# Optimization experiments

Hardware: AMD Instinct MI355X
Metric: run time of the kernel (lower is better)

## Reference

```python
import jax, jax.numpy as jnp
import numpy as np

B = 131072
D = 256
N_SC = 16
SC_CAP = 2
MAX_USERS = 8
POW_DIM = 10


def setup_inputs() -> dict:
    key = jax.random.key(0)
    k0, k1, k2, k3 = jax.random.split(key, 4)
    x = jax.random.normal(k0, (B, D), dtype=jnp.float32)
    available_actions = jax.random.randint(k1, (B, 2 * MAX_USERS), 0, 2).astype(jnp.int32)
    # per-head Categorical weights: Linear(D, action_dim), small init (gain=0.01 orthogonal-ish)
    W_sc = jax.random.normal(k2, (MAX_USERS, D, N_SC), dtype=jnp.float32) * 0.01
    b_sc = jnp.zeros((MAX_USERS, N_SC), dtype=jnp.float32)
    W_pow = jax.random.normal(k3, (MAX_USERS, D, POW_DIM), dtype=jnp.float32) * 0.01
    b_pow = jnp.zeros((MAX_USERS, POW_DIM), dtype=jnp.float32)
    return {"x": x, "available_actions": available_actions,
            "W_sc": W_sc, "b_sc": b_sc, "W_pow": W_pow, "b_pow": b_pow}


def reference(x, available_actions, W_sc, b_sc, W_pow, b_pow):
    # NOMA branch of MultiDiscreteACTLayer.forward (deterministic=False).
    Bn = x.shape[0]
    key = jax.random.key(42)
    sc_keys = jax.random.split(key, MAX_USERS)
    pow_key = jax.random.fold_in(key, 999)

    NEG = jnp.float32(-1e10)

    def sc_step(sc_stat, inp):
        W, b, avail, k = inp  # W:[D,N_SC], b:[N_SC], avail:[Bn] float, k: key
        logits = x @ W + b                       # [Bn, N_SC]
        mask = sc_stat < SC_CAP                  # subchannel still has capacity
        logits = jnp.where(mask, logits, NEG)
        action = jax.random.categorical(k, logits)        # [Bn] int
        logp = jnp.take_along_axis(jax.nn.log_softmax(logits, -1),
                                   action[:, None], axis=-1)[:, 0]
        # availability masking: unavailable -> action=-1, logp=0
        action = jnp.where(avail > 0, action, -1)
        logp = logp * avail
        # scatter: sc_stat[b, action] += 1 where action != -1
        upd = jnp.where((action >= 0)[:, None],
                        jax.nn.one_hot(jnp.maximum(action, 0), N_SC, dtype=sc_stat.dtype),
                        jnp.zeros((), sc_stat.dtype))
        return sc_stat + upd, (action, logp)

    sc_stat0 = jnp.zeros((Bn, N_SC), dtype=x.dtype)
    avail_f = available_actions.astype(x.dtype)
    avail_sc = avail_f[:, :MAX_USERS].T          # [MAX_USERS, Bn]
    _, (sc_actions, sc_logps) = jax.lax.scan(
        sc_step, sc_stat0, (W_sc, b_sc, avail_sc, sc_keys))

    # power heads: no mask, no loop-carried state -> fully batched
    pow_logits = jnp.einsum('bd,hdk->bhk', x, W_pow) + b_pow   # [Bn, H, POW_DIM]
    pow_actions = jax.random.categorical(pow_key, pow_logits)  # [Bn, H]
    pow_logps = jnp.take_along_axis(jax.nn.log_softmax(pow_logits, -1),
                                    pow_actions[..., None], axis=-1)[..., 0]
    avail_pow = avail_f[:, MAX_USERS:]
    pow_actions = jnp.where(avail_pow > 0, pow_actions, -1)
    pow_logps = pow_logps * avail_pow

    actions = jnp.concatenate([sc_actions.T, pow_actions], axis=-1)          # [Bn, 16]
    action_log_probs = jnp.concatenate([sc_logps.T, pow_logps], axis=-1)
    action_log_probs = jnp.sum(action_log_probs, axis=-1, keepdims=True)     # [Bn, 1]
    return actions, action_log_probs, available_actions
```

## Files before the change

kernel.cpp:

```cpp
#include <hip/hip_runtime.h>


#define B_TOTAL 131072
#define NCOL    208
#define ROWS    32
#define TINYF   1.17549435e-38f

#define WPLANE  53248
#define XB_L    8448
#define XB_P    264

typedef float f32x4 __attribute__((ext_vector_type(4)));
typedef short short8 __attribute__((ext_vector_type(8)));

#define MFMA_BF16(A,B,C) __builtin_amdgcn_mfma_f32_16x16x32_bf16((A),(B),(C),0,0,0)

#define ROR16(v, n) __uint_as_float((unsigned)__builtin_amdgcn_update_dpp(     \
    (int)__float_as_uint(v), (int)__float_as_uint(v), 0x120 | (n), 0xF, 0xF, false))

__device__ __forceinline__ float redmax16(float v) {
  v = fmaxf(v, ROR16(v, 8));
  v = fmaxf(v, ROR16(v, 4));
  v = fmaxf(v, ROR16(v, 2));
  v = fmaxf(v, ROR16(v, 1));
  return v;
}
__device__ __forceinline__ float redsum16(float v) {
  v += ROR16(v, 8);
  v += ROR16(v, 4);
  v += ROR16(v, 2);
  v += ROR16(v, 1);
  return v;
}

struct TF2 { unsigned a, b; };

__host__ __device__ constexpr unsigned rotl_(unsigned x, int r) {
  return (x << r) | (x >> (32 - r));
}

__host__ __device__ constexpr TF2 tf2(unsigned k0, unsigned k1, unsigned x0, unsigned x1) {
  unsigned ks0 = k0, ks1 = k1, ks2 = k0 ^ k1 ^ 0x1BD11BDAu;
  x0 += ks0; x1 += ks1;
  x0 += x1; x1 = rotl_(x1, 13); x1 ^= x0;
  x0 += x1; x1 = rotl_(x1, 15); x1 ^= x0;
  x0 += x1; x1 = rotl_(x1, 26); x1 ^= x0;
  x0 += x1; x1 = rotl_(x1,  6); x1 ^= x0;
  x0 += ks1; x1 += ks2 + 1u;
  x0 += x1; x1 = rotl_(x1, 17); x1 ^= x0;
  x0 += x1; x1 = rotl_(x1, 29); x1 ^= x0;
  x0 += x1; x1 = rotl_(x1, 16); x1 ^= x0;
  x0 += x1; x1 = rotl_(x1, 24); x1 ^= x0;
  x0 += ks2; x1 += ks0 + 2u;
  x0 += x1; x1 = rotl_(x1, 13); x1 ^= x0;
  x0 += x1; x1 = rotl_(x1, 15); x1 ^= x0;
  x0 += x1; x1 = rotl_(x1, 26); x1 ^= x0;
  x0 += x1; x1 = rotl_(x1,  6); x1 ^= x0;
  x0 += ks0; x1 += ks1 + 3u;
  x0 += x1; x1 = rotl_(x1, 17); x1 ^= x0;
  x0 += x1; x1 = rotl_(x1, 29); x1 ^= x0;
  x0 += x1; x1 = rotl_(x1, 16); x1 ^= x0;
  x0 += x1; x1 = rotl_(x1, 24); x1 ^= x0;
  x0 += ks1; x1 += ks2 + 4u;
  x0 += x1; x1 = rotl_(x1, 13); x1 ^= x0;
  x0 += x1; x1 = rotl_(x1, 15); x1 ^= x0;
  x0 += x1; x1 = rotl_(x1, 26); x1 ^= x0;
  x0 += x1; x1 = rotl_(x1,  6); x1 ^= x0;
  x0 += ks2; x1 += ks0 + 5u;
  return TF2{x0, x1};
}

__host__ __device__ constexpr unsigned key_a(unsigned d) { return tf2(0u, 42u, 0u, d).a; }
__host__ __device__ constexpr unsigned key_b(unsigned d) { return tf2(0u, 42u, 0u, d).b; }

constexpr unsigned SK0c[8] = {
  key_a(0), key_a(1), key_a(2), key_a(3), key_a(4), key_a(5), key_a(6), key_a(7)
};
constexpr unsigned SK1c[8] = {
  key_b(0), key_b(1), key_b(2), key_b(3), key_b(4), key_b(5), key_b(6), key_b(7)
};
constexpr unsigned PK0 = key_a(999);
constexpr unsigned PK1 = key_b(999);

__device__ __forceinline__ double dlog(double xd) {
  long long b = __double_as_longlong(xd);
  int e = (int)(b >> 52) - 1023;
  double m = __longlong_as_double((b & 0x000FFFFFFFFFFFFFLL) | 0x3FF0000000000000LL);
  if (m > 1.4142135623730951) { m *= 0.5; e += 1; }
  double mp1 = m + 1.0;
  double r = (double)__builtin_amdgcn_rcpf((float)mp1);
  r = fma(fma(-mp1, r, 1.0), r, r);
  double z  = (m - 1.0) * r;
  double z2 = z * z;
  double p = fma(z2, fma(z2, fma(z2, fma(z2, fma(z2,
              1.0/13.0, 1.0/11.0), 1.0/9.0), 1.0/7.0), 1.0/5.0), 1.0/3.0);
  double lm = fma(2.0 * z, z2 * p, 2.0 * z);
  return fma((double)e, 0.6931471805599453, lm);
}

__device__ __forceinline__ float gumbelf(unsigned bits) {
  float u = __uint_as_float((bits >> 9) | 0x3f800000u) - 1.0f;
  u = u + TINYF;
  u = fmaxf(TINYF, u);
  double nl = -dlog((double)u);
  return -(float)dlog(nl);
}

__global__ void repack_kernel(const float* __restrict__ Wsc, const float* __restrict__ bsc,
                              const float* __restrict__ Wpow, const float* __restrict__ bpow,
                              short* __restrict__ Wb, float* __restrict__ bp) {
  int t = blockIdx.x * 256 + threadIdx.x;
  if (t < 53248) {
    int j    = t & 7;
    int lane = (t >> 3) & 63;
    int c    = (t >> 9) & 7;
    int T    = t >> 12;
    int k    = c * 32 + (lane >> 4) * 8 + j;
    int col  = T * 16 + (lane & 15);
    int u = col / 26, n = col % 26;
    float w = (n < 16) ? Wsc[(u * 256 + k) * 16 + n]
                       : Wpow[(u * 256 + k) * 10 + (n - 16)];
    unsigned b0 = __float_as_uint(w) & 0xFFFF0000u;
    float f1 = w - __uint_as_float(b0);
    unsigned b1 = __float_as_uint(f1) & 0xFFFF0000u;
    float f2 = f1 - __uint_as_float(b1);
    unsigned b2 = __float_as_uint(f2) & 0xFFFF0000u;
    int idx = (T * 8 + c) * 512 + lane * 8 + j;
    Wb[idx]              = (short)(b0 >> 16);
    Wb[WPLANE + idx]     = (short)(b1 >> 16);
    Wb[2 * WPLANE + idx] = (short)(b2 >> 16);
  } else {
    int cc = t - 53248;
    float v = 0.f;
    if (cc < NCOL) {
      int u = cc / 26, n = cc % 26;
      v = (n < 16) ? bsc[u * 16 + n] : bpow[u * 10 + (n - 16)];
    }
    bp[cc] = v;
  }
}

#define PROD8(X0, X1, X2, W0, W1, W2, AM, AS) do {                      \
    AM = MFMA_BF16(X0, W0, AM);                                         \
    AS = MFMA_BF16(X1, W0, AS);                                         \
    AS = MFMA_BF16(X0, W1, AS);                                         \
    AS = MFMA_BF16(X1, W1, AS);                                         \
    AS = MFMA_BF16(X2, W0, AS);                                         \
    AS = MFMA_BF16(X0, W2, AS);                                         \
    AS = MFMA_BF16(X2, W1, AS);                                         \
    AS = MFMA_BF16(X1, W2, AS);                                         \
  } while (0)

__global__ __launch_bounds__(512, 4) void act_kernel(
    const float* __restrict__ x, const int* __restrict__ avail,
    const short* __restrict__ Wb, const float* __restrict__ bp,
    float* __restrict__ out) {
  __shared__ __align__(16) union SMem {
    short xb[3][ROWS][XB_P];
    float gpow[ROWS][80];
  } sm;
  __shared__ float lg[ROWS][NCOL];

  const int t = threadIdx.x;
  const int b0 = blockIdx.x * ROWS;

#pragma unroll
  for (int i = 0; i < 4; ++i) {
    int flat = t + 512 * i;
    int r  = flat >> 6;
    int kq = flat & 63;
    float4 v = ((const float4*)(x + (size_t)(b0 + r) * 256))[kq];
    unsigned L0[4], L1[4], L2[4];
#pragma unroll
    for (int e = 0; e < 4; ++e) {
      float f = (&v.x)[e];
      unsigned h0 = __float_as_uint(f) & 0xFFFF0000u;
      float f1 = f - __uint_as_float(h0);
      unsigned h1 = __float_as_uint(f1) & 0xFFFF0000u;
      float f2 = f1 - __uint_as_float(h1);
      unsigned h2 = __float_as_uint(f2) & 0xFFFF0000u;
      L0[e] = h0; L1[e] = h1; L2[e] = h2;
    }
    int ks = 4 * kq;
    *(uint2*)&sm.xb[0][r][ks] =
        make_uint2((L0[0] >> 16) | (L0[1] & 0xFFFF0000u),
                   (L0[2] >> 16) | (L0[3] & 0xFFFF0000u));
    *(uint2*)&sm.xb[1][r][ks] =
        make_uint2((L1[0] >> 16) | (L1[1] & 0xFFFF0000u),
                   (L1[2] >> 16) | (L1[3] & 0xFFFF0000u));
    *(uint2*)&sm.xb[2][r][ks] =
        make_uint2((L2[0] >> 16) | (L2[1] & 0xFFFF0000u),
                   (L2[2] >> 16) | (L2[3] & 0xFFFF0000u));
  }
  __syncthreads();

  {
    const int lane64 = t & 63;
    const int wv  = t >> 6;
    const int q   = lane64 >> 4;
    const int r16 = lane64 & 15;
    const int tA  = (wv + (blockIdx.x & 7)) & 7;
    const bool heavy = tA < 5;
    const int tB  = 8 + tA;

    const f32x4 fz = {0.f, 0.f, 0.f, 0.f};
    f32x4 mA0 = fz, sA0 = fz, mA1 = fz, sA1 = fz;
    f32x4 mB0 = fz, sB0 = fz, mB1 = fz, sB1 = fz;

    const short* xr0 = &sm.xb[0][r16][0];
    const short* xr1 = &sm.xb[0][16 + r16][0];
    const int wlane = lane64 * 8;

#pragma unroll 1
    for (int c = 0; c < 8; ++c) {
      const int xo = c * 32 + q * 8;
      short8 a0 = *(const short8*)(xr0 + xo);
      short8 a1 = *(const short8*)(xr0 + XB_L + xo);
      short8 a2 = *(const short8*)(xr0 + 2 * XB_L + xo);
      short8 c0_ = *(const short8*)(xr1 + xo);
      short8 c1_ = *(const short8*)(xr1 + XB_L + xo);
      short8 c2_ = *(const short8*)(xr1 + 2 * XB_L + xo);
      {
        const int wi = (tA * 8 + c) * 512 + wlane;
        short8 w0 = *(const short8*)(Wb + wi);
        short8 w1 = *(const short8*)(Wb + WPLANE + wi);
        short8 w2 = *(const short8*)(Wb + 2 * WPLANE + wi);
        PROD8(a0,  a1,  a2,  w0, w1, w2, mA0, sA0);
        PROD8(c0_, c1_, c2_, w0, w1, w2, mA1, sA1);
      }
      if (heavy) {
        const int wi = (tB * 8 + c) * 512 + wlane;
        short8 w0 = *(const short8*)(Wb + wi);
        short8 w1 = *(const short8*)(Wb + WPLANE + wi);
        short8 w2 = *(const short8*)(Wb + 2 * WPLANE + wi);
        PROD8(a0,  a1,  a2,  w0, w1, w2, mB0, sB0);
        PROD8(c0_, c1_, c2_, w0, w1, w2, mB1, sB1);
      }
    }

    {
      short8 pa = {0, 0, 0, 0, 0, 0, 0, 0};
      short8 pb = {0, 0, 0, 0, 0, 0, 0, 0};
      if (q == 0) {
        pa[0] = (short)(__float_as_uint((float)r16) >> 16);
        pb[0] = (short)0x3F80;
      }
      f32x4 pr = MFMA_BF16(pa, pb, fz);
      f32x4 pc = MFMA_BF16(pb, pa, fz);
#pragma unroll
      for (int r = 0; r < 4; ++r) {
        int i  = ((int)(pr[r] + 0.5f)) & 15;
        int jo = ((int)(pc[r] + 0.5f)) & 15;
        int cA = tA * 16 + jo;
        lg[i][cA]      = mA0[r] + (sA0[r] + bp[cA]);
        lg[16 + i][cA] = mA1[r] + (sA1[r] + bp[cA]);
        if (heavy) {
          int cB = tB * 16 + jo;
          lg[i][cB]      = mB0[r] + (sB0[r] + bp[cB]);
          lg[16 + i][cB] = mB1[r] + (sB1[r] + bp[cB]);
        }
      }
    }
  }

  float gsc[8];
  {
    const int prow = t >> 4;
    const int pn   = t & 15;
    const unsigned cnt = (unsigned)((b0 + prow) * 16 + pn);
#pragma unroll
    for (int u = 0; u < 8; ++u) {
      TF2 r = tf2(SK0c[u], SK1c[u], 0u, cnt);
      gsc[u] = gumbelf(r.a ^ r.b);
    }
  }
  __syncthreads();

#pragma unroll
  for (int i = 0; i < 5; ++i) {
    int flat = t + 512 * i;
    int prw  = (flat * 13108) >> 20;
    int q80  = flat - prw * 80;
    unsigned cnt = (unsigned)((b0 + prw) * 80 + q80);
    TF2 r = tf2(PK0, PK1, 0u, cnt);
    sm.gpow[prw][q80] = gumbelf(r.a ^ r.b);
  }
  __syncthreads();

  const int row  = t >> 4;
  const int lane = t & 15;
  const int g16  = (t & 63) >> 4;
  const int shamt = g16 * 16;
  const int gb   = b0 + row;
  const int av = avail[gb * 16 + lane];
  const unsigned avm = (unsigned)((__ballot(av > 0) >> shamt) & 0xFFFFull);
  int stat = 0;
  float lpsum = 0.0f;
  float my_act = 0.0f;

#pragma unroll
  for (int u = 0; u < 8; ++u) {
    float logit = lg[row][u * 26 + lane];
    float ml = (stat < 2) ? logit : -1e10f;
    float y  = ml + gsc[u];
    float vmax = redmax16(y);
    unsigned long long bal = __ballot(y == vmax);
    int idx = __builtin_ctz((unsigned)((bal >> shamt) & 0xFFFFull));
    float s = redsum16(__expf(ml));
    float mlidx = redmax16((lane == idx) ? ml : -3.0e38f);
    float lp = mlidx - __logf(s);
    int au = (int)((avm >> u) & 1u);
    if (au) {
      lpsum += lp;
      if (lane == idx) stat += 1;
    }
    if (lane == u) my_act = au ? (float)idx : -1.0f;
  }

#pragma unroll
  for (int h = 0; h < 8; ++h) {
    bool on = lane < 10;
    float logit = on ? lg[row][h * 26 + 16 + lane] : -3.0e38f;
    float y     = on ? (logit + sm.gpow[row][h * 10 + lane]) : -3.0e38f;
    float vmax = redmax16(y);
    unsigned long long bal = __ballot(y == vmax);
    int idx = __builtin_ctz((unsigned)((bal >> shamt) & 0xFFFFull));
    float s = redsum16(on ? __expf(logit) : 0.0f);
    float mlidx = redmax16((lane == idx) ? logit : -3.0e38f);
    float lp = mlidx - __logf(s);
    int ah = (int)((avm >> (8 + h)) & 1u);
    if (ah) lpsum += lp;
    if (lane == 8 + h) my_act = ah ? (float)idx : -1.0f;
  }

  out[(size_t)gb * 16 + lane] = my_act;
  if (lane == 0) out[(size_t)B_TOTAL * 16 + gb] = lpsum;
  out[(size_t)B_TOTAL * 17 + (size_t)gb * 16 + lane] = (float)av;
}

extern "C" void kernel_launch(void* const* d_in, const int* in_sizes, int n_in,
                              void* d_out, int out_size, void* d_ws, size_t ws_size,
                              hipStream_t stream) {
  const float* x    = (const float*)d_in[0];
  const int*   av   = (const int*)  d_in[1];
  const float* Wsc  = (const float*)d_in[2];
  const float* bsc  = (const float*)d_in[3];
  const float* Wpow = (const float*)d_in[4];
  const float* bpow = (const float*)d_in[5];
  float* outp = (float*)d_out;

  float* bp = (float*)d_ws;
  short* Wb = (short*)((char*)d_ws + 1024);

  repack_kernel<<<209, 256, 0, stream>>>(Wsc, bsc, Wpow, bpow, Wb, bp);
  act_kernel<<<B_TOTAL / ROWS, 512, 0, stream>>>(x, av, Wb, bp, outp);
}
```

Measured before the change: 375.9 us.

## Alias transposed logits buffer into x staging LDS and raise occupancy target

Moves the logits scratch into the same shared-memory union as the bf16 x split buffers, stored transposed so each thread writes its four MFMA accumulator rows as one float4. This removes the separate logits allocation, so more blocks can share a CU's LDS, and launch bounds are raised from 4 to 6 blocks per CU. An extra barrier is added before overwriting the x buffers, and the subchannel Gumbel noise generation is moved after the logit stores. The higher occupancy target constrains registers and may cause spills, and the transposed reads may hit bank conflicts.

```diff
diff --git a/kernel.cpp b/kernel.cpp
--- a/kernel.cpp
+++ b/kernel.cpp
@@ -9,6 +9,7 @@
 #define WPLANE  53248
 #define XB_L    8448
 #define XB_P    264
+#define LGP     36
 
 typedef float f32x4 __attribute__((ext_vector_type(4)));
 typedef short short8 __attribute__((ext_vector_type(8)));
@@ -151,15 +152,17 @@
     AS = MFMA_BF16(X1, W2, AS);                                         \
   } while (0)
 
-__global__ __launch_bounds__(512, 4) void act_kernel(
+__global__ __launch_bounds__(512, 6) void act_kernel(
     const float* __restrict__ x, const int* __restrict__ avail,
     const short* __restrict__ Wb, const float* __restrict__ bp,
     float* __restrict__ out) {
   __shared__ __align__(16) union SMem {
     short xb[3][ROWS][XB_P];
-    float gpow[ROWS][80];
+    struct {
+      float gpow[ROWS][80];
+      float lgT[NCOL][LGP];
+    } c;
   } sm;
-  __shared__ float lg[ROWS][NCOL];
 
   const int t = threadIdx.x;
   const int b0 = blockIdx.x * ROWS;
@@ -194,16 +197,18 @@
   }
   __syncthreads();
 
+  const int lane64 = t & 63;
+  const int wv  = t >> 6;
+  const int q   = lane64 >> 4;
+  const int r16 = lane64 & 15;
+  const int tA  = (wv + (blockIdx.x & 7)) & 7;
+  const bool heavy = tA < 5;
+  const int tB  = 8 + tA;
+
+  const f32x4 fz = {0.f, 0.f, 0.f, 0.f};
+  f32x4 dA0, dA1, dB0, dB1;
+  int i0, jo;
   {
-    const int lane64 = t & 63;
-    const int wv  = t >> 6;
-    const int q   = lane64 >> 4;
-    const int r16 = lane64 & 15;
-    const int tA  = (wv + (blockIdx.x & 7)) & 7;
-    const bool heavy = tA < 5;
-    const int tB  = 8 + tA;
-
-    const f32x4 fz = {0.f, 0.f, 0.f, 0.f};
     f32x4 mA0 = fz, sA0 = fz, mA1 = fz, sA1 = fz;
     f32x4 mB0 = fz, sB0 = fz, mB1 = fz, sB1 = fz;
 
@@ -238,43 +243,39 @@
       }
     }
 
-    {
-      short8 pa = {0, 0, 0, 0, 0, 0, 0, 0};
-      short8 pb = {0, 0, 0, 0, 0, 0, 0, 0};
-      if (q == 0) {
-        pa[0] = (short)(__float_as_uint((float)r16) >> 16);
-        pb[0] = (short)0x3F80;
-      }
-      f32x4 pr = MFMA_BF16(pa, pb, fz);
-      f32x4 pc = MFMA_BF16(pb, pa, fz);
-#pragma unroll
-      for (int r = 0; r < 4; ++r) {
-        int i  = ((int)(pr[r] + 0.5f)) & 15;
-        int jo = ((int)(pc[r] + 0.5f)) & 15;
-        int cA = tA * 16 + jo;
-        lg[i][cA]      = mA0[r] + (sA0[r] + bp[cA]);
-        lg[16 + i][cA] = mA1[r] + (sA1[r] + bp[cA]);
-        if (heavy) {
-          int cB = tB * 16 + jo;
-          lg[i][cB]      = mB0[r] + (sB0[r] + bp[cB]);
-          lg[16 + i][cB] = mB1[r] + (sB1[r] + bp[cB]);
-        }
-      }
-    }
-  }
-
-  float gsc[8];
+    short8 pa = {0, 0, 0, 0, 0, 0, 0, 0};
+    short8 pb = {0, 0, 0, 0, 0, 0, 0, 0};
+    if (q == 0) {
+      pa[0] = (short)(__float_as_uint((float)r16) >> 16);
+      pb[0] = (short)0x3F80;
+    }
+    f32x4 pr = MFMA_BF16(pa, pb, fz);
+    f32x4 pc = MFMA_BF16(pb, pa, fz);
+    i0 = ((int)(pr[0] + 0.5f)) & 15;
+    jo = ((int)(pc[0] + 0.5f)) & 15;
+
+    dA0 = mA0 + sA0; dA1 = mA1 + sA1;
+    dB0 = mB0 + sB0; dB1 = mB1 + sB1;
+  }
+  __syncthreads();
+
   {
-    const int prow = t >> 4;
-    const int pn   = t & 15;
-    const unsigned cnt = (unsigned)((b0 + prow) * 16 + pn);
-#pragma unroll
-    for (int u = 0; u < 8; ++u) {
-      TF2 r = tf2(SK0c[u], SK1c[u], 0u, cnt);
-      gsc[u] = gumbelf(r.a ^ r.b);
-    }
-  }
-  __syncthreads();
+    const int cA = tA * 16 + jo;
+    float bpA = bp[cA];
+    float4 v0, v1;
+    v0.x = dA0[0] + bpA; v0.y = dA0[1] + bpA; v0.z = dA0[2] + bpA; v0.w = dA0[3] + bpA;
+    v1.x = dA1[0] + bpA; v1.y = dA1[1] + bpA; v1.z = dA1[2] + bpA; v1.w = dA1[3] + bpA;
+    *(float4*)&sm.c.lgT[cA][i0]      = v0;
+    *(float4*)&sm.c.lgT[cA][16 + i0] = v1;
+    if (heavy) {
+      const int cB = tB * 16 + jo;
+      float bpB = bp[cB];
+      v0.x = dB0[0] + bpB; v0.y = dB0[1] + bpB; v0.z = dB0[2] + bpB; v0.w = dB0[3] + bpB;
+      v1.x = dB1[0] + bpB; v1.y = dB1[1] + bpB; v1.z = dB1[2] + bpB; v1.w = dB1[3] + bpB;
+      *(float4*)&sm.c.lgT[cB][i0]      = v0;
+      *(float4*)&sm.c.lgT[cB][16 + i0] = v1;
+    }
+  }
 
 #pragma unroll
   for (int i = 0; i < 5; ++i) {
@@ -283,7 +284,19 @@
     int q80  = flat - prw * 80;
     unsigned cnt = (unsigned)((b0 + prw) * 80 + q80);
     TF2 r = tf2(PK0, PK1, 0u, cnt);
-    sm.gpow[prw][q80] = gumbelf(r.a ^ r.b);
+    sm.c.gpow[prw][q80] = gumbelf(r.a ^ r.b);
+  }
+
+  float gsc[8];
+  {
+    const int prow = t >> 4;
+    const int pn   = t & 15;
+    const unsigned cnt = (unsigned)((b0 + prow) * 16 + pn);
+#pragma unroll
+    for (int u = 0; u < 8; ++u) {
+      TF2 r = tf2(SK0c[u], SK1c[u], 0u, cnt);
+      gsc[u] = gumbelf(r.a ^ r.b);
+    }
   }
   __syncthreads();
 
@@ -300,7 +313,7 @@
 
 #pragma unroll
   for (int u = 0; u < 8; ++u) {
-    float logit = lg[row][u * 26 + lane];
+    float logit = sm.c.lgT[u * 26 + lane][row];
     float ml = (stat < 2) ? logit : -1e10f;
     float y  = ml + gsc[u];
     float vmax = redmax16(y);
@@ -320,8 +333,8 @@
 #pragma unroll
   for (int h = 0; h < 8; ++h) {
     bool on = lane < 10;
-    float logit = on ? lg[row][h * 26 + 16 + lane] : -3.0e38f;
-    float y     = on ? (logit + sm.gpow[row][h * 10 + lane]) : -3.0e38f;
+    float logit = on ? sm.c.lgT[h * 26 + 16 + lane][row] : -3.0e38f;
+    float y     = on ? (logit + sm.c.gpow[row][h * 10 + lane]) : -3.0e38f;
     float vmax = redmax16(y);
     unsigned long long bal = __ballot(y == vmax);
     int idx = __builtin_ctz((unsigned)((bal >> shamt) & 0xFFFFull));
```

After: 379.2 us. No clear change (+0.9%).
